# Kernel optimization log

Hardware: AMD Instinct MI355X
Metric: run time of the kernel (lower is better)

Reference implementation:

```python
import jax, jax.numpy as jnp
import numpy as np


def setup_inputs() -> dict:
    key = jax.random.key(0)
    ks = jax.random.split(key, 8)
    B, T, C = 8, 2048, 1024
    X = jax.random.normal(ks[0], (B, T, C), dtype=jnp.float32)
    dX = jax.random.normal(ks[1], (B, T, C), dtype=jnp.float32)
    S_n = jnp.zeros((B, C), dtype=jnp.float32)
    att_mask = jnp.ones((B, T), dtype=jnp.int64)
    # parameters (torch init: randn(C,C)/C ; nn.Linear default uniform)
    W_Q = jax.random.normal(ks[2], (C, C), dtype=jnp.float32) / C
    W_K = jax.random.normal(ks[3], (C, C), dtype=jnp.float32) / C
    W_V = jax.random.normal(ks[4], (C, C), dtype=jnp.float32) / C
    bound = 1.0 / np.sqrt(C)
    W_hh = jax.random.uniform(ks[5], (C, C), minval=-bound, maxval=bound, dtype=jnp.float32)
    b_hh = jax.random.uniform(ks[6], (C,), minval=-bound, maxval=bound, dtype=jnp.float32)
    return {"X": X, "dX": dX, "S_n": S_n, "att_mask": att_mask,
            "W_Q": W_Q, "W_K": W_K, "W_V": W_V, "W_hh": W_hh, "b_hh": b_hh}


def reference(X, dX, S_n, att_mask, W_Q, W_K, W_V, W_hh, b_hh):
    B, T, C = X.shape
    # chunk_len is hard-coded to 1 in the source, so per-step:
    #   Q_t,K_t,V_t: [B,1,C]; c_t = Q_t @ K_t^T: [B,1,1]; A_t = c_t @ V_t.
    # These have no cross-timestep dependency -> precompute in parallel.
    Q = jax.nn.relu(jnp.einsum('btc,cd->btd', X, W_Q))
    K = jax.nn.relu(jnp.einsum('btc,cd->btd', X, W_K))
    V = jnp.einsum('btc,cd->btd', X, W_V)
    s = jnp.sum(Q * K, axis=-1, keepdims=True)        # [B,T,1]
    A = s * V                                          # [B,T,C]
    # A_factor = A_scale[chunk_len-1] = linspace(0,-1,ceil(T/2))[0] == 0.0
    A_scale = jnp.concatenate([jnp.linspace(0.0, -1.0, (T + 1) // 2),
                               jnp.linspace(-1.0, 0.0, T // 2)])
    A_factor = A_scale[0]

    def step(carry, A_t):
        h, prev_A = carry
        h_new = jnp.tanh(h @ W_hh.T + b_hh + A_t + prev_A * A_factor)
        return (h_new, A_t), h_new

    h0 = jnp.zeros((B, C), X.dtype)
    A_seq = jnp.swapaxes(A, 0, 1)                      # [T,B,C]
    _, H = jax.lax.scan(step, (h0, h0), A_seq)
    out = jnp.swapaxes(H, 0, 1)                        # [B,T,C]
    return out, S_n
```

## Files before the change

### kernel.cpp

```cpp
#include <hip/hip_runtime.h>
#include <hip/hip_bf16.h>

#define Bn 8
#define Tn 2048
#define Cn 1024

typedef __attribute__((ext_vector_type(8))) short short8;
typedef __attribute__((ext_vector_type(4))) float f32x4;
typedef __attribute__((ext_vector_type(4))) unsigned int u32x4;

__device__ __forceinline__ unsigned short f2bf(float x) {
    union { float f; unsigned u; } v; v.f = x;
    return (unsigned short)((v.u + 0x7FFFu + ((v.u >> 16) & 1u)) >> 16);
}

__global__ __launch_bounds__(256) void transpose_cvt(const float* __restrict__ W,
                                                     unsigned short* __restrict__ WT) {
    __shared__ float tile[64][65];
    const int bx = blockIdx.x;
    const int tr = (bx >> 4) << 6;
    const int tc = (bx & 15) << 6;
    const int tid = threadIdx.x;
    const int r  = tid >> 2;
    const int c4 = (tid & 3) << 4;
#pragma unroll
    for (int i = 0; i < 4; ++i) {
        float4 v = *(const float4*)(W + (long)(tr + r) * Cn + tc + c4 + i * 4);
        tile[r][c4 + i * 4 + 0] = v.x;
        tile[r][c4 + i * 4 + 1] = v.y;
        tile[r][c4 + i * 4 + 2] = v.z;
        tile[r][c4 + i * 4 + 3] = v.w;
    }
    __syncthreads();
    short8 p0, p1;
#pragma unroll
    for (int i = 0; i < 8; ++i)  p0[i] = (short)f2bf(tile[c4 + i][r]);
#pragma unroll
    for (int i = 0; i < 8; ++i)  p1[i] = (short)f2bf(tile[c4 + 8 + i][r]);
    unsigned short* dst = WT + (long)(tc + r) * Cn + tr + c4;
    *(short8*)(dst)     = p0;
    *(short8*)(dst + 8) = p1;
}

__global__ __launch_bounds__(256, 1) void qkv_fused(const float* __restrict__ X,
                                                    const unsigned short* __restrict__ WqT,
                                                    const unsigned short* __restrict__ WkT,
                                                    const unsigned short* __restrict__ WvT,
                                                    float* __restrict__ Aout) {
    extern __shared__ char smem[];
    char* xs = smem;
    char* b0 = smem + 131072;
    char* b1 = smem + 147456;
    const int tid = threadIdx.x;
    const long row0 = (long)blockIdx.x * 64;

#pragma unroll 4
    for (int it = 0; it < 32; ++it) {
        int chunk = it * 256 + tid;
        int r  = chunk >> 7;
        int cc = chunk & 127;
        const float* src = X + (row0 + r) * Cn + cc * 8;
        float4 v0 = *(const float4*)src;
        float4 v1 = *(const float4*)(src + 4);
        short8 p;
        p[0] = (short)f2bf(v0.x); p[1] = (short)f2bf(v0.y);
        p[2] = (short)f2bf(v0.z); p[3] = (short)f2bf(v0.w);
        p[4] = (short)f2bf(v1.x); p[5] = (short)f2bf(v1.y);
        p[6] = (short)f2bf(v1.z); p[7] = (short)f2bf(v1.w);
        *(short8*)(xs + r * 2048 + ((cc * 16) ^ ((r & 7) << 4))) = p;
    }

    const int lane = tid & 63;
    const int wv   = tid >> 6;
    const int wm   = wv & 1;
    const int wn   = wv >> 1;
    const int m0   = wm * 32;
    const int l15  = lane & 15;
    const int lk   = lane >> 4;

    float s_part[2][4] = {};

    for (int nb = 0; nb < 8; ++nb) {
        const int n0 = nb * 128;
        f32x4 qa[2][4] = {};
        f32x4 ka[2][4] = {};
        for (int k0 = 0; k0 < 16; ++k0) {
            const int kk = k0 * 64;
            __syncthreads();
#pragma unroll
            for (int i = 0; i < 4; ++i) {
                int ch = i * 256 + tid;
                int n  = ch >> 3;
                int s  = ch & 7;
                int loff = n * 128 + ((s * 16) ^ ((n & 7) << 4));
                long goff = (long)(n0 + n) * Cn + kk + s * 8;
                *(short8*)(b0 + loff) = *(const short8*)(WqT + goff);
                *(short8*)(b1 + loff) = *(const short8*)(WkT + goff);
            }
            __syncthreads();
#pragma unroll
            for (int ki = 0; ki < 2; ++ki) {
                const int kb  = (kk + ki * 32 + lk * 8) * 2;
                const int r0  = m0 + l15, r1 = m0 + 16 + l15;
                short8 a0 = *(const short8*)(xs + r0 * 2048 + (kb ^ ((r0 & 7) << 4)));
                short8 a1 = *(const short8*)(xs + r1 * 2048 + (kb ^ ((r1 & 7) << 4)));
                const int bkb = (ki * 32 + lk * 8) * 2;
#pragma unroll
                for (int nf = 0; nf < 4; ++nf) {
                    int n = wn * 64 + nf * 16 + l15;
                    int boff = n * 128 + (bkb ^ ((n & 7) << 4));
                    short8 bq = *(const short8*)(b0 + boff);
                    qa[0][nf] = __builtin_amdgcn_mfma_f32_16x16x32_bf16(a0, bq, qa[0][nf], 0, 0, 0);
                    qa[1][nf] = __builtin_amdgcn_mfma_f32_16x16x32_bf16(a1, bq, qa[1][nf], 0, 0, 0);
                    short8 bk = *(const short8*)(b1 + boff);
                    ka[0][nf] = __builtin_amdgcn_mfma_f32_16x16x32_bf16(a0, bk, ka[0][nf], 0, 0, 0);
                    ka[1][nf] = __builtin_amdgcn_mfma_f32_16x16x32_bf16(a1, bk, ka[1][nf], 0, 0, 0);
                }
            }
        }
#pragma unroll
        for (int mf = 0; mf < 2; ++mf)
#pragma unroll
            for (int nf = 0; nf < 4; ++nf)
#pragma unroll
                for (int r = 0; r < 4; ++r) {
                    float q = fmaxf(qa[mf][nf][r], 0.f);
                    float k = fmaxf(ka[mf][nf][r], 0.f);
                    s_part[mf][r] += q * k;
                }
    }
#pragma unroll
    for (int mf = 0; mf < 2; ++mf)
#pragma unroll
        for (int r = 0; r < 4; ++r) {
            float v = s_part[mf][r];
            v += __shfl_xor(v, 1);
            v += __shfl_xor(v, 2);
            v += __shfl_xor(v, 4);
            v += __shfl_xor(v, 8);
            s_part[mf][r] = v;
        }

    {
        float* s_red = (float*)b1;
        if (l15 == 0) {
#pragma unroll
            for (int mf = 0; mf < 2; ++mf)
#pragma unroll
                for (int r = 0; r < 4; ++r)
                    s_red[wn * 64 + m0 + mf * 16 + lk * 4 + r] = s_part[mf][r];
        }
        __syncthreads();
#pragma unroll
        for (int mf = 0; mf < 2; ++mf)
#pragma unroll
            for (int r = 0; r < 4; ++r) {
                int row = m0 + mf * 16 + lk * 4 + r;
                s_part[mf][r] = s_red[row] + s_red[64 + row];
            }
        __syncthreads();
    }

    for (int nb = 0; nb < 8; ++nb) {
        const int n0 = nb * 128;
        f32x4 va[2][4] = {};
        for (int k0 = 0; k0 < 16; ++k0) {
            const int kk = k0 * 64;
            __syncthreads();
#pragma unroll
            for (int i = 0; i < 4; ++i) {
                int ch = i * 256 + tid;
                int n  = ch >> 3;
                int s  = ch & 7;
                *(short8*)(b0 + n * 128 + ((s * 16) ^ ((n & 7) << 4))) =
                    *(const short8*)(WvT + (long)(n0 + n) * Cn + kk + s * 8);
            }
            __syncthreads();
#pragma unroll
            for (int ki = 0; ki < 2; ++ki) {
                const int kb  = (kk + ki * 32 + lk * 8) * 2;
                const int r0  = m0 + l15, r1 = m0 + 16 + l15;
                short8 a0 = *(const short8*)(xs + r0 * 2048 + (kb ^ ((r0 & 7) << 4)));
                short8 a1 = *(const short8*)(xs + r1 * 2048 + (kb ^ ((r1 & 7) << 4)));
                const int bkb = (ki * 32 + lk * 8) * 2;
#pragma unroll
                for (int nf = 0; nf < 4; ++nf) {
                    int n = wn * 64 + nf * 16 + l15;
                    short8 bv = *(const short8*)(b0 + n * 128 + (bkb ^ ((n & 7) << 4)));
                    va[0][nf] = __builtin_amdgcn_mfma_f32_16x16x32_bf16(a0, bv, va[0][nf], 0, 0, 0);
                    va[1][nf] = __builtin_amdgcn_mfma_f32_16x16x32_bf16(a1, bv, va[1][nf], 0, 0, 0);
                }
            }
        }
#pragma unroll
        for (int mf = 0; mf < 2; ++mf)
#pragma unroll
            for (int nf = 0; nf < 4; ++nf)
#pragma unroll
                for (int r = 0; r < 4; ++r) {
                    long row = row0 + m0 + mf * 16 + lk * 4 + r;
                    int  col = n0 + wn * 64 + nf * 16 + l15;
                    Aout[row * Cn + col] = s_part[mf][r] * va[mf][nf][r];
                }
    }
}

#define CK(tag, dat, bit, vv)                                                 \
    if ((pend & (bit)) && (tag) == expect) {                                  \
        vv = __uint_as_float(dat); pend &= ~(bit);                            \
    }

__global__ __launch_bounds__(256, 2)
void recurrence(const float* __restrict__ A,
                const float* __restrict__ Whh,
                const float* __restrict__ bhh,
                unsigned long long* __restrict__ cbuf,
                float* __restrict__ out) {
    const int tid = threadIdx.x;
    const int b   = blockIdx.x & 7;
    const int sl  = blockIdx.x >> 3;
    const int j0  = sl * 32;
    const int j   = tid & 31;
    const int ch  = tid >> 5;

    __shared__ float sbuf[16000];
    float* h_lds = sbuf;
    float* part2 = sbuf + 1024;

    float4 w[32];
    const float4* wp = (const float4*)(Whh + (long)(j0 + j) * Cn + ch * 128);
#pragma unroll
    for (int r = 0; r < 32; ++r) w[r] = wp[r];
#pragma unroll
    for (int r = 0; r < 32; ++r) {
        asm volatile("" : "+v"(w[r].x), "+v"(w[r].y), "+v"(w[r].z), "+v"(w[r].w));
    }

    const float bh = (tid < 32) ? bhh[j0 + tid] : 0.f;

    for (int t = 1; t <= Tn; ++t) {
        float a_val = 0.f;
        if (tid < 32) a_val = A[((long)b * Tn + (t - 1)) * Cn + j0 + tid];

        unsigned long long* src =
            cbuf + ((size_t)((t - 1) & 1) * Bn + b) * Cn + tid * 4;
        const unsigned expect = (unsigned)(t - 1);
        float v0 = 0.f, v1 = 0.f, v2 = 0.f, v3 = 0.f;
        unsigned pend = 0xF;
        u32x4 pa, pb;
        do {
            asm volatile(
                "global_load_dwordx4 %0, %2, off sc0\n\t"
                "global_load_dwordx4 %1, %2, off offset:16 sc0\n\t"
                "s_waitcnt vmcnt(0)"
                : "=&v"(pa), "=&v"(pb) : "v"(src) : "memory");
            CK(pa.y, pa.x, 1u, v0) CK(pa.w, pa.z, 2u, v1)
            CK(pb.y, pb.x, 4u, v2) CK(pb.w, pb.z, 8u, v3)
            if (!pend) break;
            asm volatile(
                "global_load_dwordx4 %0, %2, off sc0 sc1\n\t"
                "global_load_dwordx4 %1, %2, off offset:16 sc0 sc1\n\t"
                "s_waitcnt vmcnt(0)"
                : "=&v"(pa), "=&v"(pb) : "v"(src) : "memory");
            CK(pa.y, pa.x, 1u, v0) CK(pa.w, pa.z, 2u, v1)
            CK(pb.y, pb.x, 4u, v2) CK(pb.w, pb.z, 8u, v3)
        } while (pend);

        *(float4*)(h_lds + tid * 4) = make_float4(v0, v1, v2, v3);
        asm volatile("s_waitcnt lgkmcnt(0)" ::: "memory");
        __builtin_amdgcn_sched_barrier(0);

        float ax = 0.f, ay = 0.f, az = 0.f, aw = 0.f;
#pragma unroll
        for (int r = 0; r < 32; ++r) {
            float4 h4 = *(const float4*)(h_lds + ch * 128 + r * 4);
            ax = fmaf(w[r].x, h4.x, ax);
            ay = fmaf(w[r].y, h4.y, ay);
            az = fmaf(w[r].z, h4.z, az);
            aw = fmaf(w[r].w, h4.w, aw);
        }
        part2[(t & 1) * 256 + ch * 32 + j] = (ax + ay) + (az + aw);
        __syncthreads();

        if (tid < 32) {
            const float* pp = part2 + (t & 1) * 256;
            float s = ((pp[tid] + pp[32 + tid]) + (pp[64 + tid] + pp[96 + tid])) +
                      ((pp[128 + tid] + pp[160 + tid]) + (pp[192 + tid] + pp[224 + tid]));
            float x = s + a_val + bh;
            float e = __expf(x + x);
            float ht = 1.f - 2.f * __builtin_amdgcn_rcpf(e + 1.f);
            unsigned long long pk =
                ((unsigned long long)(unsigned)t << 32) | (unsigned long long)__float_as_uint(ht);
            unsigned long long* dst =
                cbuf + ((size_t)(t & 1) * Bn + b) * Cn + j0 + tid;
            asm volatile(
                "global_store_dwordx2 %0, %1, off sc0\n\t"
                "global_store_dwordx2 %0, %1, off sc0 sc1"
                :: "v"(dst), "v"(pk) : "memory");
            out[((long)b * Tn + (t - 1)) * Cn + j0 + tid] = ht;
        }
    }
}

extern "C" void kernel_launch(void* const* d_in, const int* in_sizes, int n_in,
                              void* d_out, int out_size, void* d_ws, size_t ws_size,
                              hipStream_t stream) {
    const float* X   = (const float*)d_in[0];
    const float* S_n = (const float*)d_in[2];
    const float* W_Q = (const float*)d_in[4];
    const float* W_K = (const float*)d_in[5];
    const float* W_V = (const float*)d_in[6];
    const float* Whh = (const float*)d_in[7];
    const float* bhh = (const float*)d_in[8];
    float* out = (float*)d_out;

    char* ws = (char*)d_ws;
    float*              A     = (float*)ws;
    unsigned short*     WqT   = (unsigned short*)(ws + 67108864);
    unsigned short*     WkT   = WqT + 1024 * 1024;
    unsigned short*     WvT   = WkT + 1024 * 1024;
    unsigned long long* cbuf  = (unsigned long long*)(ws + 67108864 + 3 * 2097152);

    (void)hipFuncSetAttribute((const void*)qkv_fused,
                              hipFuncAttributeMaxDynamicSharedMemorySize, 163840);

    (void)hipMemsetAsync(cbuf, 0, 2 * Bn * Cn * sizeof(unsigned long long), stream);

    transpose_cvt<<<256, 256, 0, stream>>>(W_Q, WqT);
    transpose_cvt<<<256, 256, 0, stream>>>(W_K, WkT);
    transpose_cvt<<<256, 256, 0, stream>>>(W_V, WvT);

    qkv_fused<<<256, 256, 163840, stream>>>(X, WqT, WkT, WvT, A);

    recurrence<<<256, 256, 0, stream>>>(A, Whh, bhh, cbuf, out);

    (void)hipMemcpyAsync(out + (long)Bn * Tn * Cn, S_n, Bn * Cn * sizeof(float),
                         hipMemcpyDeviceToDevice, stream);
}
```

Before: 4.581 ms.

## Assign recurrence roles per XCD so each batch stays on one chiplet

The recurrence now launches 512 blocks and has each block read its hardware XCC id and claim one of 32 slots on that XCD through atomic counters. This maps each batch's 32 column slices onto a single chiplet, so the per-step exchange of hidden state stays in that XCD's L2 and avoids cross-die traffic. Blocks that arrive after their XCD is full wait until all 512 have checked in, then take any slots still free on other XCDs, and blocks with no role exit. The added cost is an atomic claim phase at kernel start plus a spin-wait, and it relies on all 512 blocks being resident together, with two blocks per CU.

```diff
diff --git a/kernel.cpp b/kernel.cpp
--- a/kernel.cpp
+++ b/kernel.cpp
@@ -215,17 +215,56 @@
                 const float* __restrict__ Whh,
                 const float* __restrict__ bhh,
                 unsigned long long* __restrict__ cbuf,
+                unsigned int* __restrict__ claim,
                 float* __restrict__ out) {
     const int tid = threadIdx.x;
-    const int b   = blockIdx.x & 7;
-    const int sl  = blockIdx.x >> 3;
+
+    __shared__ float sbuf[16000];
+    float* h_lds = sbuf;
+    float* part2 = sbuf + 1024;
+    __shared__ int s_role;
+
+    if (tid == 0) {
+        unsigned xcd;
+        asm volatile("s_getreg_b32 %0, hwreg(HW_REG_XCC_ID)" : "=s"(xcd));
+        xcd &= 7u;
+        unsigned slot = __hip_atomic_fetch_add(claim + xcd, 1u,
+                                               __ATOMIC_RELAXED, __HIP_MEMORY_SCOPE_AGENT);
+        int role = -1;
+        if (slot < 32u) {
+            role = (int)(xcd * 32u + slot);
+            (void)__hip_atomic_fetch_add(claim + 8, 1u,
+                                         __ATOMIC_RELAXED, __HIP_MEMORY_SCOPE_AGENT);
+        } else {
+            (void)__hip_atomic_fetch_add(claim + 8, 1u,
+                                         __ATOMIC_RELAXED, __HIP_MEMORY_SCOPE_AGENT);
+            while (__hip_atomic_load(claim + 8, __ATOMIC_RELAXED,
+                                     __HIP_MEMORY_SCOPE_AGENT) < 512u) {
+            }
+            unsigned c[8];
+            for (int x = 0; x < 8; ++x)
+                c[x] = __hip_atomic_load(claim + x, __ATOMIC_RELAXED,
+                                         __HIP_MEMORY_SCOPE_AGENT);
+            unsigned myov = __hip_atomic_fetch_add(claim + 9, 1u,
+                                                   __ATOMIC_RELAXED, __HIP_MEMORY_SCOPE_AGENT);
+            unsigned acc = 0;
+            for (int x = 0; x < 8 && role < 0; ++x) {
+                unsigned freeX = (c[x] < 32u) ? (32u - c[x]) : 0u;
+                if (myov < acc + freeX)
+                    role = x * 32 + (int)(32u - freeX + (myov - acc));
+                acc += freeX;
+            }
+        }
+        s_role = role;
+    }
+    __syncthreads();
+    const int role = s_role;
+    if (role < 0) return;
+    const int b   = role >> 5;
+    const int sl  = role & 31;
     const int j0  = sl * 32;
     const int j   = tid & 31;
     const int ch  = tid >> 5;
-
-    __shared__ float sbuf[16000];
-    float* h_lds = sbuf;
-    float* part2 = sbuf + 1024;
 
     float4 w[32];
     const float4* wp = (const float4*)(Whh + (long)(j0 + j) * Cn + ch * 128);
@@ -320,11 +359,13 @@
     unsigned short*     WkT   = WqT + 1024 * 1024;
     unsigned short*     WvT   = WkT + 1024 * 1024;
     unsigned long long* cbuf  = (unsigned long long*)(ws + 67108864 + 3 * 2097152);
+    unsigned int*       claim = (unsigned int*)(ws + 67108864 + 3 * 2097152 + 131072);
 
     (void)hipFuncSetAttribute((const void*)qkv_fused,
                               hipFuncAttributeMaxDynamicSharedMemorySize, 163840);
 
     (void)hipMemsetAsync(cbuf, 0, 2 * Bn * Cn * sizeof(unsigned long long), stream);
+    (void)hipMemsetAsync(claim, 0, 10 * sizeof(unsigned int), stream);
 
     transpose_cvt<<<256, 256, 0, stream>>>(W_Q, WqT);
     transpose_cvt<<<256, 256, 0, stream>>>(W_K, WkT);
@@ -332,7 +373,7 @@
 
     qkv_fused<<<256, 256, 163840, stream>>>(X, WqT, WkT, WvT, A);
 
-    recurrence<<<256, 256, 0, stream>>>(A, Whh, bhh, cbuf, out);
+    recurrence<<<512, 256, 0, stream>>>(A, Whh, bhh, cbuf, claim, out);
 
     (void)hipMemcpyAsync(out + (long)Bn * Tn * Cn, S_n, Bn * Cn * sizeof(float),
                          hipMemcpyDeviceToDevice, stream);
```

New measurement: 4.813 ms. 1.05x slower.
